# Performance work log

Hardware: AMD Instinct MI355X
Metric: run time of the kernel (lower is better)

Reference implementation:

```python
import jax, jax.numpy as jnp
import numpy as np


def setup_inputs() -> dict:
    key = jax.random.key(0)
    kx, kt = jax.random.split(key)
    b, n, d = 4, 4096, 1024
    x = jax.random.normal(kx, (b, n, d), dtype=jnp.float32)
    t = jax.random.normal(kt, (n, d), dtype=jnp.float32)
    return {"x": x, "t": t}


def reference(x, t):
    # y[b,i,d] = sum_{j<=i} t[i-j,d] * x[b,j,d]
    # Causal depthwise Toeplitz matvec == linear convolution truncated to n.
    # Computed via FFT along the sequence axis (zero-pad to 2n so the
    # circular convolution equals the linear one on the first n outputs).
    b, n, d = x.shape
    L = 2 * n
    xf = jnp.fft.rfft(x.astype(jnp.float32), n=L, axis=1)        # (b, L/2+1, d) complex
    tf = jnp.fft.rfft(t.astype(jnp.float32), n=L, axis=0)        # (L/2+1, d) complex
    y = jnp.fft.irfft(xf * tf[None], n=L, axis=1)[:, :n, :]      # (b, n, d)
    return y.astype(x.dtype)
```

## Files before the change

### kernel.cpp

```cpp
#include <hip/hip_runtime.h>

#define NT 512
#define SCL (1.0f / 8192.0f)
#define PI_F 3.14159265358979323846f

__device__ __forceinline__ int P(int i) { return i ^ ((i >> 5) & 31); }

__device__ __forceinline__ float2 cmul(float2 a, float2 b) {
  return make_float2(a.x * b.x - a.y * b.y, a.x * b.y + a.y * b.x);
}
__device__ __forceinline__ float2 csqr(float2 a) {
  return make_float2(a.x * a.x - a.y * a.y, 2.f * a.x * a.y);
}
__device__ __forceinline__ float2 cadd(float2 a, float2 b) { return make_float2(a.x + b.x, a.y + b.y); }
__device__ __forceinline__ float2 csub(float2 a, float2 b) { return make_float2(a.x - b.x, a.y - b.y); }
__device__ __forceinline__ float2 cmuli (float2 a) { return make_float2(-a.y,  a.x); }
__device__ __forceinline__ float2 cmulmi(float2 a) { return make_float2( a.y, -a.x); }

constexpr float RT2 = 0.70710678118654752440f;
constexpr float CQ1 = 0.92387953251128675613f;
constexpr float SQ1 = 0.38268343236508977173f;
constexpr float C8x[4] = {1.f,  RT2, 0.f, -RT2};
constexpr float C8y[4] = {0.f, -RT2, -1.f, -RT2};
constexpr float C16x[8] = {1.f,  CQ1,  RT2,  SQ1, 0.f, -SQ1, -RT2, -CQ1};
constexpr float C16y[8] = {0.f, -SQ1, -RT2, -CQ1, -1.f, -CQ1, -RT2, -SQ1};

template<bool UNIT>
__device__ __forceinline__ void r8_fwd(float2* e, float2 b) {
  float2 b2, b4;
  if (!UNIT) { b2 = csqr(b); b4 = csqr(b2); }
  #pragma unroll
  for (int j = 0; j < 4; ++j) {
    float2 u = e[j], v = e[j + 4];
    float2 d = csub(u, v);
    e[j] = cadd(u, v);
    float2 c8 = make_float2(C8x[j], C8y[j]);
    if (UNIT) e[j + 4] = (j == 0) ? d : cmul(d, c8);
    else      e[j + 4] = cmul(d, (j == 0) ? b : cmul(b, c8));
  }
  #pragma unroll
  for (int o = 0; o < 8; o += 4) {
    #pragma unroll
    for (int j = 0; j < 2; ++j) {
      float2 u = e[o + j], v = e[o + j + 2];
      float2 d = csub(u, v);
      e[o + j] = cadd(u, v);
      if (UNIT) e[o + j + 2] = (j == 0) ? d : cmulmi(d);
      else      e[o + j + 2] = cmul(d, (j == 0) ? b2 : cmulmi(b2));
    }
  }
  #pragma unroll
  for (int o = 0; o < 8; o += 2) {
    float2 u = e[o], v = e[o + 1];
    float2 d = csub(u, v);
    e[o] = cadd(u, v);
    e[o + 1] = UNIT ? d : cmul(d, b4);
  }
}

template<bool UNIT>
__device__ __forceinline__ void r8_inv(float2* e, float2 g) {
  float2 g2, g4;
  if (!UNIT) { g2 = csqr(g); g4 = csqr(g2); }
  #pragma unroll
  for (int o = 0; o < 8; o += 2) {
    float2 t = UNIT ? e[o + 1] : cmul(e[o + 1], g4);
    float2 u = e[o];
    e[o] = cadd(u, t); e[o + 1] = csub(u, t);
  }
  #pragma unroll
  for (int o = 0; o < 8; o += 4) {
    #pragma unroll
    for (int j = 0; j < 2; ++j) {
      float2 v = e[o + j + 2];
      float2 t;
      if (UNIT) t = (j == 0) ? v : cmuli(v);
      else      t = cmul(v, (j == 0) ? g2 : cmuli(g2));
      float2 u = e[o + j];
      e[o + j] = cadd(u, t); e[o + j + 2] = csub(u, t);
    }
  }
  #pragma unroll
  for (int j = 0; j < 4; ++j) {
    float2 v = e[j + 4];
    float2 t;
    float2 c8c = make_float2(C8x[j], -C8y[j]);
    if (UNIT) t = (j == 0) ? v : cmul(v, c8c);
    else      t = cmul(v, (j == 0) ? g : cmul(g, c8c));
    float2 u = e[j];
    e[j] = cadd(u, t); e[j + 4] = csub(u, t);
  }
}

__device__ __forceinline__ void t8f(float2* cb, int base, int G, float2 b) {
  float2 e[8];
  #pragma unroll
  for (int j = 0; j < 8; ++j) e[j] = cb[P(base + G * j)];
  r8_fwd<false>(e, b);
  #pragma unroll
  for (int j = 0; j < 8; ++j) cb[P(base + G * j)] = e[j];
}

__device__ __forceinline__ void t8i(float2* cb, int base, int G, float2 g) {
  float2 e[8];
  #pragma unroll
  for (int j = 0; j < 8; ++j) e[j] = cb[P(base + G * j)];
  r8_inv<false>(e, g);
  #pragma unroll
  for (int j = 0; j < 8; ++j) cb[P(base + G * j)] = e[j];
}

__global__ __launch_bounds__(NT)
void that8h(const float* __restrict__ tT, float2* __restrict__ ThG) {
  __shared__ float2 cb[8192];
  const int tid = threadIdx.x;
  const int d = blockIdx.x;

  const int baseB = ((tid >> 6) << 9) + (tid & 63);
  const int baseC = ((tid >> 3) << 6) + (tid & 7);

  float s0, c0; __sincosf(-PI_F * (float)tid / 2048.f, &s0, &c0);
  const float2 bA = make_float2(c0, s0);
  float s1, c1; __sincosf(-PI_F * (float)(tid & 63) / 256.f, &s1, &c1);
  const float2 bB = make_float2(c1, s1);
  float s2, c2; __sincosf(-PI_F * (float)(tid & 7) / 32.f, &s2, &c2);
  const float2 bC = make_float2(c2, s2);
  float sw, cw; __sincosf(-PI_F * (float)tid / 4096.f, &sw, &cw);
  const float2 whi = make_float2(cw, sw);

  const float* tp = tT + (size_t)d * 4096;
  {
    float2 tv[8];
    #pragma unroll
    for (int j = 0; j < 8; ++j) tv[j] = make_float2(tp[tid + 512 * j], 0.f);
    float2 e[8];
    #pragma unroll
    for (int j = 0; j < 8; ++j) e[j] = tv[j];
    r8_fwd<false>(e, bA);
    #pragma unroll
    for (int j = 0; j < 8; ++j) cb[P(tid + 512 * j)] = e[j];
    #pragma unroll
    for (int j = 0; j < 8; ++j) {
      float2 w = (j == 0) ? whi : cmul(whi, make_float2(C16x[j], C16y[j]));
      e[j] = make_float2(tv[j].x * w.x, tv[j].x * w.y);
    }
    r8_fwd<false>(e, bA);
    #pragma unroll
    for (int j = 0; j < 8; ++j) cb[P(4096 + tid + 512 * j)] = e[j];
  }
  __syncthreads();
  t8f(cb, baseB, 64, bB);
  t8f(cb, 4096 + baseB, 64, bB);
  __syncthreads();
  t8f(cb, baseC, 8, bC);
  t8f(cb, 4096 + baseC, 8, bC);
  __syncthreads();
  float2* thg = ThG + (size_t)d * 2 * 4096;
  #pragma unroll 1
  for (int h = 0; h < 2; ++h) {
    float2 e[8];
    #pragma unroll
    for (int j = 0; j < 8; ++j) e[j] = cb[P(h * 4096 + tid * 8 + j)];
    r8_fwd<true>(e, make_float2(1.f, 0.f));
    #pragma unroll
    for (int j = 0; j < 8; ++j)
      thg[h * 4096 + tid + 512 * j] = make_float2(e[j].x * SCL, e[j].y * SCL);
  }
}

__global__ __launch_bounds__(NT)
void fftconv(float* __restrict__ xT, const float2* __restrict__ ThG) {
  __shared__ float2 cb[8192];
  const int tid = threadIdx.x;
  const int d = blockIdx.x;
  const int pass = blockIdx.y;

  const int baseB = ((tid >> 6) << 9) + (tid & 63);
  const int baseC = ((tid >> 3) << 6) + (tid & 7);
  const int baseM = tid << 3;
  const float2 ONE = make_float2(1.f, 0.f);

  float s0, c0; __sincosf(-PI_F * (float)tid / 2048.f, &s0, &c0);
  const float2 bA = make_float2(c0, s0);
  const float2 gA = make_float2(c0, -s0);
  float s1, c1; __sincosf(-PI_F * (float)(tid & 63) / 256.f, &s1, &c1);
  const float2 bB = make_float2(c1, s1);
  const float2 gB = make_float2(c1, -s1);
  float s2, c2; __sincosf(-PI_F * (float)(tid & 7) / 32.f, &s2, &c2);
  const float2 bC = make_float2(c2, s2);
  const float2 gC = make_float2(c2, -s2);
  float sw, cw; __sincosf(-PI_F * (float)tid / 4096.f, &sw, &cw);
  const float2 whi  = make_float2(cw, sw);
  const float2 whic = make_float2(cw, -sw);

  float* r0 = xT + ((size_t)(2 * pass)     * 1024 + d) * 4096;
  float* r1 = xT + ((size_t)(2 * pass + 1) * 1024 + d) * 4096;
  const float2* thl = ThG + (size_t)d * 2 * 4096;
  const float2* thh = thl + 4096;

  {
    float2 xv[8];
    #pragma unroll
    for (int j = 0; j < 8; ++j) {
      int n = tid + 512 * j;
      xv[j] = make_float2(r0[n], r1[n]);
    }
    float2 e[8];
    #pragma unroll
    for (int j = 0; j < 8; ++j) e[j] = xv[j];
    r8_fwd<false>(e, bA);
    #pragma unroll
    for (int j = 0; j < 8; ++j) cb[P(tid + 512 * j)] = e[j];
    #pragma unroll
    for (int j = 0; j < 8; ++j) {
      float2 w = (j == 0) ? whi : cmul(whi, make_float2(C16x[j], C16y[j]));
      e[j] = cmul(xv[j], w);
    }
    r8_fwd<false>(e, bA);
    #pragma unroll
    for (int j = 0; j < 8; ++j) cb[P(4096 + tid + 512 * j)] = e[j];
  }
  __syncthreads();

  float2 thL[8], thH[8];
  #pragma unroll
  for (int j = 0; j < 8; ++j) thL[j] = thl[tid + 512 * j];
  #pragma unroll
  for (int j = 0; j < 8; ++j) thH[j] = thh[tid + 512 * j];
  t8f(cb, baseB, 64, bB);
  t8f(cb, 4096 + baseB, 64, bB);
  __syncthreads();

  t8f(cb, baseC, 8, bC);
  t8f(cb, 4096 + baseC, 8, bC);
  __syncthreads();

  #pragma unroll 1
  for (int h = 0; h < 2; ++h) {
    float2 e[8];
    #pragma unroll
    for (int j = 0; j < 8; ++j) e[j] = cb[P(h * 4096 + baseM + j)];
    r8_fwd<true>(e, ONE);
    #pragma unroll
    for (int j = 0; j < 8; ++j) e[j] = cmul(e[j], h ? thH[j] : thL[j]);
    r8_inv<true>(e, ONE);
    #pragma unroll
    for (int j = 0; j < 8; ++j) cb[P(h * 4096 + baseM + j)] = e[j];
  }
  __syncthreads();

  t8i(cb, baseC, 8, gC);
  t8i(cb, 4096 + baseC, 8, gC);
  __syncthreads();

  t8i(cb, baseB, 64, gB);
  t8i(cb, 4096 + baseB, 64, gB);
  __syncthreads();

  {
    float2 u[8], v[8];
    #pragma unroll
    for (int j = 0; j < 8; ++j) u[j] = cb[P(tid + 512 * j)];
    r8_inv<false>(u, gA);
    #pragma unroll
    for (int j = 0; j < 8; ++j) v[j] = cb[P(4096 + tid + 512 * j)];
    r8_inv<false>(v, gA);
    #pragma unroll
    for (int k = 0; k < 8; ++k) {
      float2 wc = (k == 0) ? whic : cmul(whic, make_float2(C16x[k], -C16y[k]));
      float2 t = cmul(v[k], wc);
      int n = tid + 512 * k;
      r0[n] = u[k].x + t.x;
      r1[n] = u[k].y + t.y;
    }
  }
}

__global__ __launch_bounds__(256)
void transpose64(const float* __restrict__ src, float* __restrict__ dst, int R, int C) {
  __shared__ float tile[64][65];
  int t  = threadIdx.x;
  int c4 = t & 15;
  int r  = t >> 4;
  size_t slab = (size_t)blockIdx.z * (size_t)R * (size_t)C;
  const float* s = src + slab;
  float* dd = dst + slab;
  int col0 = blockIdx.x * 64, row0 = blockIdx.y * 64;
  #pragma unroll
  for (int k = 0; k < 4; ++k) {
    int rr = r + 16 * k;
    const float4 v = *(const float4*)(s + (size_t)(row0 + rr) * C + col0 + 4 * c4);
    tile[rr][4 * c4 + 0] = v.x;
    tile[rr][4 * c4 + 1] = v.y;
    tile[rr][4 * c4 + 2] = v.z;
    tile[rr][4 * c4 + 3] = v.w;
  }
  __syncthreads();
  #pragma unroll
  for (int k = 0; k < 4; ++k) {
    int cc = r + 16 * k;
    float4 w;
    w.x = tile[4 * c4 + 0][cc];
    w.y = tile[4 * c4 + 1][cc];
    w.z = tile[4 * c4 + 2][cc];
    w.w = tile[4 * c4 + 3][cc];
    *(float4*)(dd + (size_t)(col0 + cc) * R + row0 + 4 * c4) = w;
  }
}

extern "C" void kernel_launch(void* const* d_in, const int* in_sizes, int n_in,
                              void* d_out, int out_size, void* d_ws, size_t ws_size,
                              hipStream_t stream) {
  const float* x = (const float*)d_in[0];
  const float* t = (const float*)d_in[1];
  float* out = (float*)d_out;
  float* ws  = (float*)d_ws;
  float* xT  = ws;
  float* tT  = ws + (size_t)4 * 1024 * 4096;
  float2* ThG = (float2*)d_out;

  transpose64<<<dim3(16, 64, 4), 256, 0, stream>>>(x, xT, 4096, 1024);
  transpose64<<<dim3(16, 64, 1), 256, 0, stream>>>(t, tT, 4096, 1024);

  that8h<<<dim3(1024), NT, 0, stream>>>(tT, ThG);
  fftconv<<<dim3(1024, 2), NT, 0, stream>>>(xT, ThG);

  transpose64<<<dim3(64, 16, 4), 256, 0, stream>>>(xT, out, 1024, 4096);
}
```

Before: 152.5 us.

## Interleave even/odd half-FFTs into float4 LDS layout and fuse radix-8 passes

Stores the two 4096-point half FFTs (the plain and the twisted halves) side by side as float4 in shared memory, so each LDS access moves 16 bytes and the lo/hi radix-8 butterflies run together in one pass. The spectrum buffer ThG gets the same interleaved float4 layout, and its loads are moved later, between the radix-8 stages. This is meant to halve LDS instruction count and raise ILP per pass. In exchange it raises register pressure, and the float4 accesses may hit different LDS bank-conflict patterns under the existing P() swizzle.

```diff
diff --git a/kernel.cpp b/kernel.cpp
--- a/kernel.cpp
+++ b/kernel.cpp
@@ -92,27 +92,39 @@
   }
 }
 
-__device__ __forceinline__ void t8f(float2* cb, int base, int G, float2 b) {
-  float2 e[8];
-  #pragma unroll
-  for (int j = 0; j < 8; ++j) e[j] = cb[P(base + G * j)];
-  r8_fwd<false>(e, b);
-  #pragma unroll
-  for (int j = 0; j < 8; ++j) cb[P(base + G * j)] = e[j];
-}
-
-__device__ __forceinline__ void t8i(float2* cb, int base, int G, float2 g) {
-  float2 e[8];
-  #pragma unroll
-  for (int j = 0; j < 8; ++j) e[j] = cb[P(base + G * j)];
-  r8_inv<false>(e, g);
-  #pragma unroll
-  for (int j = 0; j < 8; ++j) cb[P(base + G * j)] = e[j];
+__device__ __forceinline__ void d8f(float4* cb, int base, int G, float2 b) {
+  float2 lo[8], hi[8];
+  #pragma unroll
+  for (int j = 0; j < 8; ++j) {
+    float4 q = cb[P(base + G * j)];
+    lo[j] = make_float2(q.x, q.y);
+    hi[j] = make_float2(q.z, q.w);
+  }
+  r8_fwd<false>(lo, b);
+  r8_fwd<false>(hi, b);
+  #pragma unroll
+  for (int j = 0; j < 8; ++j)
+    cb[P(base + G * j)] = make_float4(lo[j].x, lo[j].y, hi[j].x, hi[j].y);
+}
+
+__device__ __forceinline__ void d8i(float4* cb, int base, int G, float2 g) {
+  float2 lo[8], hi[8];
+  #pragma unroll
+  for (int j = 0; j < 8; ++j) {
+    float4 q = cb[P(base + G * j)];
+    lo[j] = make_float2(q.x, q.y);
+    hi[j] = make_float2(q.z, q.w);
+  }
+  r8_inv<false>(lo, g);
+  r8_inv<false>(hi, g);
+  #pragma unroll
+  for (int j = 0; j < 8; ++j)
+    cb[P(base + G * j)] = make_float4(lo[j].x, lo[j].y, hi[j].x, hi[j].y);
 }
 
 __global__ __launch_bounds__(NT)
-void that8h(const float* __restrict__ tT, float2* __restrict__ ThG) {
-  __shared__ float2 cb[8192];
+void that8h(const float* __restrict__ tT, float4* __restrict__ ThG) {
+  __shared__ float4 cb[4096];
   const int tid = threadIdx.x;
   const int d = blockIdx.x;
 
@@ -130,54 +142,52 @@
 
   const float* tp = tT + (size_t)d * 4096;
   {
-    float2 tv[8];
-    #pragma unroll
-    for (int j = 0; j < 8; ++j) tv[j] = make_float2(tp[tid + 512 * j], 0.f);
-    float2 e[8];
-    #pragma unroll
-    for (int j = 0; j < 8; ++j) e[j] = tv[j];
-    r8_fwd<false>(e, bA);
-    #pragma unroll
-    for (int j = 0; j < 8; ++j) cb[P(tid + 512 * j)] = e[j];
-    #pragma unroll
-    for (int j = 0; j < 8; ++j) {
+    float tv[8];
+    #pragma unroll
+    for (int j = 0; j < 8; ++j) tv[j] = tp[tid + 512 * j];
+    float2 lo[8], hi[8];
+    #pragma unroll
+    for (int j = 0; j < 8; ++j) {
+      lo[j] = make_float2(tv[j], 0.f);
       float2 w = (j == 0) ? whi : cmul(whi, make_float2(C16x[j], C16y[j]));
-      e[j] = make_float2(tv[j].x * w.x, tv[j].x * w.y);
-    }
-    r8_fwd<false>(e, bA);
-    #pragma unroll
-    for (int j = 0; j < 8; ++j) cb[P(4096 + tid + 512 * j)] = e[j];
-  }
-  __syncthreads();
-  t8f(cb, baseB, 64, bB);
-  t8f(cb, 4096 + baseB, 64, bB);
-  __syncthreads();
-  t8f(cb, baseC, 8, bC);
-  t8f(cb, 4096 + baseC, 8, bC);
-  __syncthreads();
-  float2* thg = ThG + (size_t)d * 2 * 4096;
-  #pragma unroll 1
-  for (int h = 0; h < 2; ++h) {
-    float2 e[8];
-    #pragma unroll
-    for (int j = 0; j < 8; ++j) e[j] = cb[P(h * 4096 + tid * 8 + j)];
-    r8_fwd<true>(e, make_float2(1.f, 0.f));
+      hi[j] = make_float2(tv[j] * w.x, tv[j] * w.y);
+    }
+    r8_fwd<false>(lo, bA);
+    r8_fwd<false>(hi, bA);
     #pragma unroll
     for (int j = 0; j < 8; ++j)
-      thg[h * 4096 + tid + 512 * j] = make_float2(e[j].x * SCL, e[j].y * SCL);
+      cb[P(tid + 512 * j)] = make_float4(lo[j].x, lo[j].y, hi[j].x, hi[j].y);
+  }
+  __syncthreads();
+  d8f(cb, baseB, 64, bB);  __syncthreads();
+  d8f(cb, baseC, 8, bC);   __syncthreads();
+  {
+    float2 lo[8], hi[8];
+    #pragma unroll
+    for (int j = 0; j < 8; ++j) {
+      float4 q = cb[P(tid * 8 + j)];
+      lo[j] = make_float2(q.x, q.y);
+      hi[j] = make_float2(q.z, q.w);
+    }
+    r8_fwd<true>(lo, make_float2(1.f, 0.f));
+    r8_fwd<true>(hi, make_float2(1.f, 0.f));
+    float4* thg = ThG + (size_t)d * 4096;
+    #pragma unroll
+    for (int j = 0; j < 8; ++j)
+      thg[tid + 512 * j] = make_float4(lo[j].x * SCL, lo[j].y * SCL,
+                                       hi[j].x * SCL, hi[j].y * SCL);
   }
 }
 
 __global__ __launch_bounds__(NT)
-void fftconv(float* __restrict__ xT, const float2* __restrict__ ThG) {
-  __shared__ float2 cb[8192];
+void fftconv(float* __restrict__ xT, const float4* __restrict__ ThG) {
+  __shared__ float4 cb[4096];
   const int tid = threadIdx.x;
   const int d = blockIdx.x;
   const int pass = blockIdx.y;
 
   const int baseB = ((tid >> 6) << 9) + (tid & 63);
   const int baseC = ((tid >> 3) << 6) + (tid & 7);
-  const int baseM = tid << 3;
   const float2 ONE = make_float2(1.f, 0.f);
 
   float s0, c0; __sincosf(-PI_F * (float)tid / 2048.f, &s0, &c0);
@@ -195,75 +205,75 @@
 
   float* r0 = xT + ((size_t)(2 * pass)     * 1024 + d) * 4096;
   float* r1 = xT + ((size_t)(2 * pass + 1) * 1024 + d) * 4096;
-  const float2* thl = ThG + (size_t)d * 2 * 4096;
-  const float2* thh = thl + 4096;
-
-  {
-    float2 xv[8];
+  const float4* thg = ThG + (size_t)d * 4096;
+
+  {
+    float2 xv[8], m[8];
     #pragma unroll
     for (int j = 0; j < 8; ++j) {
       int n = tid + 512 * j;
       xv[j] = make_float2(r0[n], r1[n]);
     }
-    float2 e[8];
-    #pragma unroll
-    for (int j = 0; j < 8; ++j) e[j] = xv[j];
-    r8_fwd<false>(e, bA);
-    #pragma unroll
-    for (int j = 0; j < 8; ++j) cb[P(tid + 512 * j)] = e[j];
     #pragma unroll
     for (int j = 0; j < 8; ++j) {
       float2 w = (j == 0) ? whi : cmul(whi, make_float2(C16x[j], C16y[j]));
-      e[j] = cmul(xv[j], w);
-    }
-    r8_fwd<false>(e, bA);
-    #pragma unroll
-    for (int j = 0; j < 8; ++j) cb[P(4096 + tid + 512 * j)] = e[j];
-  }
-  __syncthreads();
-
-  float2 thL[8], thH[8];
-  #pragma unroll
-  for (int j = 0; j < 8; ++j) thL[j] = thl[tid + 512 * j];
-  #pragma unroll
-  for (int j = 0; j < 8; ++j) thH[j] = thh[tid + 512 * j];
-  t8f(cb, baseB, 64, bB);
-  t8f(cb, 4096 + baseB, 64, bB);
-  __syncthreads();
-
-  t8f(cb, baseC, 8, bC);
-  t8f(cb, 4096 + baseC, 8, bC);
-  __syncthreads();
-
-  #pragma unroll 1
-  for (int h = 0; h < 2; ++h) {
-    float2 e[8];
-    #pragma unroll
-    for (int j = 0; j < 8; ++j) e[j] = cb[P(h * 4096 + baseM + j)];
-    r8_fwd<true>(e, ONE);
-    #pragma unroll
-    for (int j = 0; j < 8; ++j) e[j] = cmul(e[j], h ? thH[j] : thL[j]);
-    r8_inv<true>(e, ONE);
-    #pragma unroll
-    for (int j = 0; j < 8; ++j) cb[P(h * 4096 + baseM + j)] = e[j];
-  }
-  __syncthreads();
-
-  t8i(cb, baseC, 8, gC);
-  t8i(cb, 4096 + baseC, 8, gC);
-  __syncthreads();
-
-  t8i(cb, baseB, 64, gB);
-  t8i(cb, 4096 + baseB, 64, gB);
+      m[j] = cmul(xv[j], w);
+    }
+    r8_fwd<false>(xv, bA);
+    r8_fwd<false>(m, bA);
+    #pragma unroll
+    for (int j = 0; j < 8; ++j)
+      cb[P(tid + 512 * j)] = make_float4(xv[j].x, xv[j].y, m[j].x, m[j].y);
+  }
+  __syncthreads();
+
+  d8f(cb, baseB, 64, bB);
+  __syncthreads();
+
+  float4 thq[8];
+  #pragma unroll
+  for (int j = 0; j < 8; ++j) thq[j] = thg[tid + 512 * j];
+  d8f(cb, baseC, 8, bC);
+  __syncthreads();
+
+  {
+    float2 lo[8], hi[8];
+    #pragma unroll
+    for (int j = 0; j < 8; ++j) {
+      float4 q = cb[P(tid * 8 + j)];
+      lo[j] = make_float2(q.x, q.y);
+      hi[j] = make_float2(q.z, q.w);
+    }
+    r8_fwd<true>(lo, ONE);
+    r8_fwd<true>(hi, ONE);
+    #pragma unroll
+    for (int j = 0; j < 8; ++j) {
+      lo[j] = cmul(lo[j], make_float2(thq[j].x, thq[j].y));
+      hi[j] = cmul(hi[j], make_float2(thq[j].z, thq[j].w));
+    }
+    r8_inv<true>(lo, ONE);
+    r8_inv<true>(hi, ONE);
+    #pragma unroll
+    for (int j = 0; j < 8; ++j)
+      cb[P(tid * 8 + j)] = make_float4(lo[j].x, lo[j].y, hi[j].x, hi[j].y);
+  }
+  __syncthreads();
+
+  d8i(cb, baseC, 8, gC);
+  __syncthreads();
+
+  d8i(cb, baseB, 64, gB);
   __syncthreads();
 
   {
     float2 u[8], v[8];
     #pragma unroll
-    for (int j = 0; j < 8; ++j) u[j] = cb[P(tid + 512 * j)];
+    for (int j = 0; j < 8; ++j) {
+      float4 q = cb[P(tid + 512 * j)];
+      u[j] = make_float2(q.x, q.y);
+      v[j] = make_float2(q.z, q.w);
+    }
     r8_inv<false>(u, gA);
-    #pragma unroll
-    for (int j = 0; j < 8; ++j) v[j] = cb[P(4096 + tid + 512 * j)];
     r8_inv<false>(v, gA);
     #pragma unroll
     for (int k = 0; k < 8; ++k) {
@@ -317,7 +327,7 @@
   float* ws  = (float*)d_ws;
   float* xT  = ws;
   float* tT  = ws + (size_t)4 * 1024 * 4096;
-  float2* ThG = (float2*)d_out;
+  float4* ThG = (float4*)d_out;
 
   transpose64<<<dim3(16, 64, 4), 256, 0, stream>>>(x, xT, 4096, 1024);
   transpose64<<<dim3(16, 64, 1), 256, 0, stream>>>(t, tT, 4096, 1024);
```

Result: faster. 147.9 us (-3.0%).
